# Optimization experiments

Measured on AMD Instinct MI355X. Metric: run time of the kernel, lower is better.

## Reference

```python
import jax, jax.numpy as jnp
import numpy as np

B, S, WIDTH, M = 2, 240, 128, 20
PAD = 16


def setup_inputs() -> dict:
    key = jax.random.key(0)
    ks = jax.random.split(key, 10)
    scale = 1.0 / (WIDTH * WIDTH)
    inp = {
        "x": jax.random.normal(ks[0], (B, S, S, 3), jnp.float32),
        "fc0_w": jax.random.normal(ks[1], (5, WIDTH), jnp.float32) * 0.1,
        "fc0_b": jnp.zeros((WIDTH,), jnp.float32),
        # 5 spectral layers, complex weights stored as [..., 2] = (real, imag)
        "spec_w1": jax.random.uniform(ks[2], (5, WIDTH, WIDTH, M, M, 2), jnp.float32) * scale,
        "spec_w2": jax.random.uniform(ks[3], (5, WIDTH, WIDTH, M, M, 2), jnp.float32) * scale,
        # 5 residual 1x1 convs
        "w_w": jax.random.normal(ks[4], (5, WIDTH, WIDTH), jnp.float32) / np.sqrt(WIDTH),
        "w_b": jnp.zeros((5, WIDTH), jnp.float32),
        "fc1_w": jax.random.normal(ks[5], (WIDTH, WIDTH), jnp.float32) / np.sqrt(WIDTH),
        "fc1_b": jnp.zeros((WIDTH,), jnp.float32),
        # 4 heads (u, v, p, T): width->64->1
        "head1_w": jax.random.normal(ks[6], (4, WIDTH, 64), jnp.float32) / np.sqrt(WIDTH),
        "head1_b": jnp.zeros((4, 64), jnp.float32),
        "head2_w": jax.random.normal(ks[7], (4, 64, 1), jnp.float32) / 8.0,
        "head2_b": jnp.zeros((4, 1), jnp.float32),
    }
    return inp


def _spectral_conv(h, w1, w2):
    # h: (B, C, H, W) real; w1, w2: (C_in, C_out, M, M) complex64
    Hh, Ww = h.shape[-2], h.shape[-1]
    ft = jnp.fft.rfft2(h)  # (B, C, H, W//2+1)
    o1 = jnp.einsum('bixy,ioxy->boxy', ft[:, :, :M, :M], w1)
    o2 = jnp.einsum('bixy,ioxy->boxy', ft[:, :, -M:, :M], w2)
    out_ft = jnp.zeros((h.shape[0], w1.shape[1], Hh, Ww // 2 + 1), jnp.complex64)
    out_ft = out_ft.at[:, :, :M, :M].set(o1).at[:, :, -M:, :M].set(o2)
    return jnp.fft.irfft2(out_ft, s=(Hh, Ww))


def reference(x, fc0_w, fc0_b, spec_w1, spec_w2, w_w, w_b, fc1_w, fc1_b,
              head1_w, head1_b, head2_w, head2_b):
    Bn, sx, sy = x.shape[0], x.shape[1], x.shape[2]
    gx = jnp.broadcast_to(jnp.linspace(0.0, 1.0, sx, dtype=x.dtype)[None, :, None, None], (Bn, sx, sy, 1))
    gy = jnp.broadcast_to(jnp.linspace(0.0, 1.0, sy, dtype=x.dtype)[None, None, :, None], (Bn, sx, sy, 1))
    x1 = jnp.concatenate([x, gx, gy], axis=-1)          # (B, S, S, 5)
    h = x1 @ fc0_w + fc0_b                              # lift -> (B, S, S, width)
    h = jnp.transpose(h, (0, 3, 1, 2))                  # (B, width, S, S)
    h = jnp.pad(h, ((0, 0), (0, 0), (0, PAD), (0, PAD)))
    c1 = spec_w1[..., 0] + 1j * spec_w1[..., 1]
    c2 = spec_w2[..., 0] + 1j * spec_w2[..., 1]
    for i in range(5):
        s = _spectral_conv(h, c1[i], c2[i])
        lin = jnp.einsum('bchw,oc->bohw', h, w_w[i]) + w_b[i][None, :, None, None]
        h = s + lin
        if i < 4:
            h = jax.nn.gelu(h, approximate=False)
    h = h[..., :-PAD, :-PAD]
    h = jnp.transpose(h, (0, 2, 3, 1))                  # (B, S, S, width)
    h = jax.nn.gelu(h @ fc1_w + fc1_b, approximate=False)
    h1 = jax.nn.gelu(jnp.einsum('bhwc,kcd->kbhwd', h, head1_w)
                     + head1_b[:, None, None, None, :], approximate=False)
    out = jnp.einsum('kbhwd,kdo->kbhwo', h1, head2_w) + head2_b[:, None, None, None, :]
    return (out[0], out[1], out[2], out[3])  # u, v, p, T each (B, S, S, 1)
```

## Files before the change

kernel.cpp:

```cpp
#include <hip/hip_runtime.h>
#include <math.h>


#define SZ_H   (2ull*256*256*128)
#define O_HA   0ull
#define O_HB   (O_HA + SZ_H)
#define O_G    (O_HB + SZ_H)
#define SZ_G   (2ull*256*20*128*2)
#define O_FTT  (O_G + SZ_G)
#define SZ_FT  (2ull*40*20*128*2)
#define O_OFT  (O_FTT + SZ_FT)
#define O_EY   (O_OFT + SZ_FT)
#define SZ_EY  (256ull*20*2)
#define O_EX   (O_EY + SZ_EY)
#define SZ_EX  (256ull*40*2)
#define O_EXI  (O_EX + SZ_EX)
#define O_WWT  (O_EXI + SZ_EX)
#define SZ_WWT 81920ull
#define O_PART (O_WWT + SZ_WWT)
#define SZ_PART (8ull*204800*2)

static __device__ __forceinline__ float gelu_f(float v) {
    return 0.5f * v * (1.0f + erff(v * 0.70710678118654752f));
}

__global__ void k_prep(const float* __restrict__ w_w, float* __restrict__ ws) {
    int i = blockIdx.x * 256 + threadIdx.x;
    const float STEP = 6.2831853071795864769f / 256.0f;
    if (i < 5120) {
        int ky = i % 20, y = i / 20;
        int t = (ky * y) & 255;
        float th = t * STEP;
        ws[O_EY + 2*(size_t)i]     = cosf(th);
        ws[O_EY + 2*(size_t)i + 1] = -sinf(th);
    } else if (i < 15360) {
        int m = i - 5120; int j = m % 40, x = m / 40;
        int kx = (j < 20) ? j : (216 + j);
        int t = (kx * x) & 255;
        float th = t * STEP;
        ws[O_EX + 2*(size_t)m]     = cosf(th);
        ws[O_EX + 2*(size_t)m + 1] = -sinf(th);
    } else if (i < 25600) {
        int m = i - 15360; int j = m % 40, x = m / 40;
        int kx = (j < 20) ? j : (216 + j);
        int t = (kx * x) & 255;
        float th = t * STEP;
        ws[O_EXI + 2*(size_t)m]     = cosf(th);
        ws[O_EXI + 2*(size_t)m + 1] = sinf(th);
    } else {
        int m = i - 25600;
        if (m < 81920) {
            int l = m >> 14, r = m & 16383;
            int ic = r >> 7, oc = r & 127;
            ws[O_WWT + m] = w_w[(size_t)l*16384 + oc*128 + ic];
        }
    }
}

__global__ __launch_bounds__(256) void k_fc0(const float* __restrict__ xin,
        const float* __restrict__ w, const float* __restrict__ bv,
        float4* __restrict__ H4) {
    size_t e = (size_t)blockIdx.x * 256 + threadIdx.x;
    int c4 = (int)(e & 31) * 4;
    int y = (int)((e >> 5) & 255);
    int x = (int)((e >> 13) & 255);
    int b = (int)(e >> 21);
    float4 h = make_float4(0.f, 0.f, 0.f, 0.f);
    if (x < 240 && y < 240) {
        const float* xp = xin + (((size_t)(b*240 + x))*240 + y)*3;
        float x0 = xp[0], x1 = xp[1], x2 = xp[2];
        float gx = x*(1.0f/239.0f), gy = y*(1.0f/239.0f);
        float4 w0 = *(const float4*)&w[c4];
        float4 w1 = *(const float4*)&w[128 + c4];
        float4 w2 = *(const float4*)&w[256 + c4];
        float4 w3 = *(const float4*)&w[384 + c4];
        float4 w4 = *(const float4*)&w[512 + c4];
        float4 bb = *(const float4*)&bv[c4];
        h.x = bb.x + x0*w0.x + x1*w1.x + x2*w2.x + gx*w3.x + gy*w4.x;
        h.y = bb.y + x0*w0.y + x1*w1.y + x2*w2.y + gx*w3.y + gy*w4.y;
        h.z = bb.z + x0*w0.z + x1*w1.z + x2*w2.z + gx*w3.z + gy*w4.z;
        h.w = bb.w + x0*w0.w + x1*w1.w + x2*w2.w + gx*w3.w + gy*w4.w;
    }
    H4[e] = h;
}

__global__ __launch_bounds__(256) void k_ydft(const float* __restrict__ H,
        const float* __restrict__ Ey, float2* __restrict__ G) {
    int kh = blockIdx.x & 1;
    int x  = (blockIdx.x >> 1) & 255;
    int b  = blockIdx.x >> 9;
    int c = threadIdx.x & 127;
    int yq = __builtin_amdgcn_readfirstlane((int)(threadIdx.x >> 7));
    int k0 = kh * 10;
    const float* Hrow = H + ((size_t)(b*256 + x)) * 256 * 128;
    float ar[10], ai[10];
    #pragma unroll
    for (int k = 0; k < 10; k++) { ar[k] = 0.f; ai[k] = 0.f; }
    #pragma unroll 2
    for (int i = 0; i < 128; i++) {
        int y = yq*128 + i;
        float v = Hrow[(size_t)y*128 + c];
        const float* e = Ey + (size_t)y*40 + k0*2;
        #pragma unroll
        for (int k = 0; k < 10; k++) {
            ar[k] = fmaf(v, e[2*k],   ar[k]);
            ai[k] = fmaf(v, e[2*k+1], ai[k]);
        }
    }
    __shared__ float red[10][128][2];
    if (yq == 1) {
        #pragma unroll
        for (int k = 0; k < 10; k++) { red[k][c][0] = ar[k]; red[k][c][1] = ai[k]; }
    }
    __syncthreads();
    if (yq == 0) {
        float2* Gp = G + ((size_t)(b*256 + x))*20*128;
        #pragma unroll
        for (int k = 0; k < 10; k++)
            Gp[(k0 + k)*128 + c] = make_float2(ar[k] + red[k][c][0], ai[k] + red[k][c][1]);
    }
}

__global__ __launch_bounds__(256) void k_xdft(const float2* __restrict__ G,
        const float* __restrict__ Ex, float2* __restrict__ ftT) {
    int t = blockIdx.x;
    int ch = t & 3, jq = (t >> 2) & 3, ky = (t >> 4) % 20, b = t / 320;
    int cl = threadIdx.x & 31;
    int xq = threadIdx.x >> 5;
    int c = ch*32 + cl;
    int j0 = jq*10;
    float ar[10], ai[10];
    #pragma unroll
    for (int k = 0; k < 10; k++) { ar[k] = 0.f; ai[k] = 0.f; }
    for (int i = 0; i < 32; i++) {
        int x = xq*32 + i;
        float2 g = G[(((size_t)(b*256 + x))*20 + ky)*128 + c];
        const float2* e2 = (const float2*)(Ex + (size_t)x*80) + j0;
        #pragma unroll
        for (int k = 0; k < 10; k++) {
            float2 e = e2[k];
            ar[k] = fmaf(g.x, e.x, fmaf(-g.y, e.y, ar[k]));
            ai[k] = fmaf(g.x, e.y, fmaf( g.y, e.x, ai[k]));
        }
    }
    #pragma unroll
    for (int k = 0; k < 10; k++) {
        ar[k] += __shfl_xor(ar[k], 32);
        ai[k] += __shfl_xor(ai[k], 32);
    }
    __shared__ float red[3][10][32][2];
    int wid = threadIdx.x >> 6;
    int sub = threadIdx.x & 63;
    if (wid > 0 && sub < 32) {
        #pragma unroll
        for (int k = 0; k < 10; k++) { red[wid-1][k][cl][0] = ar[k]; red[wid-1][k][cl][1] = ai[k]; }
    }
    __syncthreads();
    if (wid == 0 && sub < 32) {
        #pragma unroll
        for (int k = 0; k < 10; k++) {
            float rr = ar[k], ii = ai[k];
            #pragma unroll
            for (int q = 0; q < 3; q++) { rr += red[q][k][cl][0]; ii += red[q][k][cl][1]; }
            ftT[((size_t)c*2 + b)*800 + (size_t)(j0 + k)*20 + ky] = make_float2(rr, ii);
        }
    }
}

__global__ __launch_bounds__(448) void k_modemix(const float2* __restrict__ w1,
        const float2* __restrict__ w2, const float2* __restrict__ ftT,
        float2* __restrict__ outp, int ic_per) {
    int bid = blockIdx.x & 255;
    int icq = blockIdx.x >> 8;
    int oc = bid >> 1;
    int mh = bid & 1;
    int tid = threadIdx.x;
    if (tid >= 400) return;
    int wsel = tid / 200;
    int m = mh*200 + (tid % 200);
    int jk = wsel*400 + m;
    const float2* wb = wsel ? w2 : w1;
    int ic0 = icq * ic_per;
    float ar0=0.f, ai0=0.f, ar1=0.f, ai1=0.f;
    #pragma unroll 8
    for (int i = 0; i < ic_per; i++) {
        int ic = ic0 + i;
        float2 wv = wb[((size_t)(ic*128 + oc))*400 + m];
        float2 f0 = ftT[(size_t)ic*1600 + jk];
        float2 f1 = ftT[(size_t)ic*1600 + 800 + jk];
        ar0 = fmaf(f0.x, wv.x, fmaf(-f0.y, wv.y, ar0));
        ai0 = fmaf(f0.x, wv.y, fmaf( f0.y, wv.x, ai0));
        ar1 = fmaf(f1.x, wv.x, fmaf(-f1.y, wv.y, ar1));
        ai1 = fmaf(f1.x, wv.y, fmaf( f1.y, wv.x, ai1));
    }
    float2* o = outp + (size_t)icq * 204800;
    o[(size_t)jk*128 + oc]         = make_float2(ar0, ai0);
    o[(size_t)(800 + jk)*128 + oc] = make_float2(ar1, ai1);
}

__global__ __launch_bounds__(512) void k_modered(const float2* __restrict__ part,
        float2* __restrict__ oft) {
    int i = blockIdx.x * 512 + threadIdx.x;
    if (i >= 204800) return;
    float2 s = part[i];
    #pragma unroll
    for (int q = 1; q < 8; q++) {
        float2 p = part[(size_t)q*204800 + i];
        s.x += p.x; s.y += p.y;
    }
    oft[i] = s;
}

__global__ __launch_bounds__(256) void k_xidft(const float2* __restrict__ oft,
        const float* __restrict__ Exi, float2* __restrict__ T) {
    int kh = blockIdx.x & 1;
    int x  = (blockIdx.x >> 1) & 255;
    int b  = blockIdx.x >> 9;
    int oc = threadIdx.x & 127;
    int js = __builtin_amdgcn_readfirstlane((int)(threadIdx.x >> 7));
    int k0 = kh * 10;
    float ar[10], ai[10];
    #pragma unroll
    for (int k = 0; k < 10; k++) { ar[k] = 0.f; ai[k] = 0.f; }
    const float2* ob = oft + (size_t)b*800*128;
    for (int j = js*20; j < js*20 + 20; j++) {
        float er = Exi[(size_t)x*80 + 2*j], ei = Exi[(size_t)x*80 + 2*j + 1];
        #pragma unroll
        for (int k = 0; k < 10; k++) {
            float2 o = ob[(size_t)(j*20 + k0 + k)*128 + oc];
            ar[k] = fmaf(o.x, er, fmaf(-o.y, ei, ar[k]));
            ai[k] = fmaf(o.x, ei, fmaf( o.y, er, ai[k]));
        }
    }
    __shared__ float red[10][128][2];
    if (js == 1) {
        #pragma unroll
        for (int k = 0; k < 10; k++) { red[k][oc][0] = ar[k]; red[k][oc][1] = ai[k]; }
    }
    __syncthreads();
    if (js == 0) {
        float2* Tp = T + ((size_t)(b*256 + x))*20*128;
        #pragma unroll
        for (int k = 0; k < 10; k++)
            Tp[(k0 + k)*128 + oc] = make_float2(ar[k] + red[k][oc][0], ai[k] + red[k][oc][1]);
    }
}

__global__ __launch_bounds__(256) void k_spec_lin(const float* __restrict__ H,
        const float2* __restrict__ T, const float* __restrict__ wwT,
        const float* __restrict__ wb, float* __restrict__ Hout, int do_gelu) {
    int yg = blockIdx.x & 3;
    int x  = (blockIdx.x >> 2) & 255;
    int b  = blockIdx.x >> 10;
    int tid = threadIdx.x;
    int lane = tid & 63;
    int wv = __builtin_amdgcn_readfirstlane(tid >> 6);
    int oc0 = wv * 32;
    int y0 = yg * 64;
    __shared__ float hl[64][132];
    const float* Hbase = H + (((size_t)(b*256 + x))*256 + y0)*128;
    #pragma unroll
    for (int it = 0; it < 8; it++) {
        int i = tid + it*256;
        int pi = i >> 5, c4 = (i & 31)*4;
        float4 v = *(const float4*)&Hbase[(size_t)pi*128 + c4];
        *(float4*)&hl[pi][c4] = v;
    }
    __syncthreads();
    float acc[32];
    #pragma unroll
    for (int o = 0; o < 32; o++) acc[o] = 0.f;
    for (int icb = 0; icb < 128; icb += 16) {
        float tvals[16];
        #pragma unroll
        for (int q = 0; q < 4; q++)
            *(float4*)&tvals[q*4] = *(const float4*)&hl[lane][icb + q*4];
        #pragma unroll
        for (int ii = 0; ii < 16; ii++) {
            float t = tvals[ii];
            const float* wr = &wwT[(size_t)(icb + ii)*128 + oc0];
            #pragma unroll
            for (int o4 = 0; o4 < 8; o4++) {
                float4 w = *(const float4*)&wr[o4*4];
                acc[o4*4]   = fmaf(t, w.x, acc[o4*4]);
                acc[o4*4+1] = fmaf(t, w.y, acc[o4*4+1]);
                acc[o4*4+2] = fmaf(t, w.z, acc[o4*4+2]);
                acc[o4*4+3] = fmaf(t, w.w, acc[o4*4+3]);
            }
        }
    }
    float csr[20], csi[20];
    {
        int y = y0 + lane;
        #pragma unroll
        for (int k = 0; k < 20; k++) {
            int t = (k * y) & 255;
            float th = t * (6.2831853071795864769f/256.0f);
            float f = (k == 0 ? 1.0f : 2.0f) * (1.0f/65536.0f);
            csr[k] = f * __cosf(th);
            csi[k] = f * __sinf(th);
        }
    }
    const float2* Tp = T + ((size_t)(b*256 + x))*20*128 + oc0;
    for (int k = 0; k < 20; k++) {
        const float2* tr = Tp + (size_t)k*128;
        float cr = csr[k], ci = csi[k];
        #pragma unroll
        for (int o = 0; o < 32; o++) {
            float2 tv = tr[o];
            acc[o] = fmaf(tv.x, cr, fmaf(-tv.y, ci, acc[o]));
        }
    }
    __syncthreads();
    const float* bp = &wb[oc0];
    #pragma unroll
    for (int o4 = 0; o4 < 8; o4++) {
        float4 r;
        r.x = acc[o4*4]   + bp[o4*4];
        r.y = acc[o4*4+1] + bp[o4*4+1];
        r.z = acc[o4*4+2] + bp[o4*4+2];
        r.w = acc[o4*4+3] + bp[o4*4+3];
        if (do_gelu) { r.x = gelu_f(r.x); r.y = gelu_f(r.y); r.z = gelu_f(r.z); r.w = gelu_f(r.w); }
        *(float4*)&hl[lane][oc0 + o4*4] = r;
    }
    __syncthreads();
    float* Obase = Hout + (((size_t)(b*256 + x))*256 + y0)*128;
    #pragma unroll
    for (int it = 0; it < 32; it++) {
        int i = tid + it*256;
        int pi = i >> 7, c = i & 127;
        Obase[(size_t)pi*128 + c] = hl[pi][c];
    }
}

__global__ __launch_bounds__(512) void k_tail(const float* __restrict__ H,
        const float* __restrict__ fc1_w, const float* __restrict__ fc1_b,
        const float* __restrict__ h1w, const float* __restrict__ h1b,
        const float* __restrict__ h2w, const float* __restrict__ h2b,
        float* __restrict__ out) {
    int tid = threadIdx.x;
    int lane = tid & 63;
    int wv = __builtin_amdgcn_readfirstlane(tid >> 6);
    int p0 = blockIdx.x * 64;
    __shared__ float smem[64*132];
    __shared__ float red[4][64];
    float (*hl)[132] = (float (*)[132])smem;
    #pragma unroll
    for (int it = 0; it < 4; it++) {
        int i = tid + it*512;
        int pi = i >> 5, c4 = (i & 31)*4;
        int p = p0 + pi;
        int bb = p / 57600, r = p % 57600;
        int xx = r / 240, yy = r % 240;
        float4 v = *(const float4*)&H[(((size_t)(bb*256 + xx))*256 + yy)*128 + c4];
        *(float4*)&hl[pi][c4] = v;
    }
    __syncthreads();
    int oc0 = wv * 16;
    float acc[16];
    #pragma unroll
    for (int o = 0; o < 16; o++) acc[o] = 0.f;
    for (int icb = 0; icb < 128; icb += 16) {
        float tvals[16];
        #pragma unroll
        for (int q = 0; q < 4; q++)
            *(float4*)&tvals[q*4] = *(const float4*)&hl[lane][icb + q*4];
        #pragma unroll
        for (int ii = 0; ii < 16; ii++) {
            float t = tvals[ii];
            const float* wr = &fc1_w[(size_t)(icb + ii)*128 + oc0];
            #pragma unroll
            for (int o4 = 0; o4 < 4; o4++) {
                float4 w = *(const float4*)&wr[o4*4];
                acc[o4*4]   = fmaf(t, w.x, acc[o4*4]);
                acc[o4*4+1] = fmaf(t, w.y, acc[o4*4+1]);
                acc[o4*4+2] = fmaf(t, w.z, acc[o4*4+2]);
                acc[o4*4+3] = fmaf(t, w.w, acc[o4*4+3]);
            }
        }
    }
    __syncthreads();
    #pragma unroll
    for (int o4 = 0; o4 < 4; o4++) {
        float4 bb = *(const float4*)&fc1_b[oc0 + o4*4];
        float4 r;
        r.x = gelu_f(acc[o4*4]   + bb.x);
        r.y = gelu_f(acc[o4*4+1] + bb.y);
        r.z = gelu_f(acc[o4*4+2] + bb.z);
        r.w = gelu_f(acc[o4*4+3] + bb.w);
        *(float4*)&hl[lane][oc0 + o4*4] = r;
    }
    __syncthreads();
    int k    = wv >> 1;
    int half = wv & 1;
    int d0 = half * 32;
    float a2[32];
    #pragma unroll
    for (int d = 0; d < 32; d++) a2[d] = 0.f;
    const float* wk = h1w + (size_t)k*8192 + d0;
    for (int cb = 0; cb < 128; cb += 8) {
        float tvals[8];
        *(float4*)&tvals[0] = *(const float4*)&hl[lane][cb];
        *(float4*)&tvals[4] = *(const float4*)&hl[lane][cb + 4];
        #pragma unroll
        for (int cc = 0; cc < 8; cc++) {
            float t = tvals[cc];
            const float* wr = &wk[(cb + cc)*64];
            #pragma unroll
            for (int d4 = 0; d4 < 8; d4++) {
                float4 w = *(const float4*)&wr[d4*4];
                a2[d4*4]   = fmaf(t, w.x, a2[d4*4]);
                a2[d4*4+1] = fmaf(t, w.y, a2[d4*4+1]);
                a2[d4*4+2] = fmaf(t, w.z, a2[d4*4+2]);
                a2[d4*4+3] = fmaf(t, w.w, a2[d4*4+3]);
            }
        }
    }
    const float* b1 = &h1b[k*64 + d0];
    const float* w2 = &h2w[k*64 + d0];
    float ph = 0.f;
    #pragma unroll
    for (int d = 0; d < 32; d++)
        ph += gelu_f(a2[d] + b1[d]) * w2[d];
    if (half == 1) red[k][lane] = ph;
    __syncthreads();
    if (half == 0)
        out[(size_t)k*115200 + p0 + lane] = ph + red[k][lane] + h2b[k];
}

extern "C" void kernel_launch(void* const* d_in, const int* in_sizes, int n_in,
                              void* d_out, int out_size, void* d_ws, size_t ws_size,
                              hipStream_t stream) {
    const float* x       = (const float*)d_in[0];
    const float* fc0_w   = (const float*)d_in[1];
    const float* fc0_b   = (const float*)d_in[2];
    const float* spec_w1 = (const float*)d_in[3];
    const float* spec_w2 = (const float*)d_in[4];
    const float* w_w     = (const float*)d_in[5];
    const float* w_b     = (const float*)d_in[6];
    const float* fc1_w   = (const float*)d_in[7];
    const float* fc1_b   = (const float*)d_in[8];
    const float* head1_w = (const float*)d_in[9];
    const float* head1_b = (const float*)d_in[10];
    const float* head2_w = (const float*)d_in[11];
    const float* head2_b = (const float*)d_in[12];
    float* ws = (float*)d_ws;
    float* out = (float*)d_out;

    int split = ws_size >= (size_t)(O_PART + SZ_PART) * 4 ? 1 : 0;

    k_prep<<<420, 256, 0, stream>>>(w_w, ws);
    k_fc0<<<16384, 256, 0, stream>>>(x, fc0_w, fc0_b, (float4*)(ws + O_HA));

    float* cur = ws + O_HA;
    float* nxt = ws + O_HB;
    float2* G    = (float2*)(ws + O_G);
    float2* ftT  = (float2*)(ws + O_FTT);
    float2* oft  = (float2*)(ws + O_OFT);
    float2* part = (float2*)(ws + O_PART);

    for (int l = 0; l < 5; l++) {
        k_ydft<<<1024, 256, 0, stream>>>(cur, ws + O_EY, G);
        k_xdft<<<640, 256, 0, stream>>>(G, ws + O_EX, ftT);
        const float2* w1l = (const float2*)(spec_w1 + (size_t)l*13107200);
        const float2* w2l = (const float2*)(spec_w2 + (size_t)l*13107200);
        if (split) {
            k_modemix<<<2048, 448, 0, stream>>>(w1l, w2l, ftT, part, 16);
            k_modered<<<400, 512, 0, stream>>>(part, oft);
        } else {
            k_modemix<<<256, 448, 0, stream>>>(w1l, w2l, ftT, oft, 128);
        }
        k_xidft<<<1024, 256, 0, stream>>>(oft, ws + O_EXI, G);
        k_spec_lin<<<2048, 256, 0, stream>>>(cur, G, ws + O_WWT + (size_t)l*16384,
                                             w_b + l*128, nxt, (l < 4) ? 1 : 0);
        float* t = cur; cur = nxt; nxt = t;
    }
    k_tail<<<1800, 512, 0, stream>>>(cur, fc1_w, fc1_b, head1_w, head1_b,
                                     head2_w, head2_b, out);
}
```

Measured before the change: 1.726 ms.

## Restructure ydft, spec_lin and tail kernels with LDS-staged twiddles and swizzled transposes

The y-DFT kernel now stages its twiddle table in shared memory and has each thread handle two channels over four y-quarters, adding a two-step shared-memory reduction and writing float4 results. The spectral+linear kernel moves to 512 threads. It stores the input tile transposed in shared memory with an XOR swizzle, so each thread owns one output channel across 16 positions and reads one weight per input channel instead of float4 weight vectors. It also reuses the precomputed Ey table for inverse-y twiddles instead of computing sin/cos, and writes results directly from registers. The tail kernel gets the same swizzled transpose plus a shuffle-based head reduction, trading more shared-memory traffic and extra barriers for fewer global weight loads and better coalescing.

```diff
diff --git a/kernel.cpp b/kernel.cpp
--- a/kernel.cpp
+++ b/kernel.cpp
@@ -22,6 +22,10 @@
 
 static __device__ __forceinline__ float gelu_f(float v) {
     return 0.5f * v * (1.0f + erff(v * 0.70710678118654752f));
+}
+
+static __device__ __forceinline__ int SWZ(int row, int col) {
+    return (row << 6) | ((((col >> 2) ^ ((row >> 2) & 15)) << 2) | (col & 3));
 }
 
 __global__ void k_prep(const float* __restrict__ w_w, float* __restrict__ ws) {
@@ -89,35 +93,66 @@
     int kh = blockIdx.x & 1;
     int x  = (blockIdx.x >> 1) & 255;
     int b  = blockIdx.x >> 9;
-    int c = threadIdx.x & 127;
-    int yq = __builtin_amdgcn_readfirstlane((int)(threadIdx.x >> 7));
+    int lane = threadIdx.x & 63;
+    int yq = __builtin_amdgcn_readfirstlane((int)(threadIdx.x >> 6));
     int k0 = kh * 10;
-    const float* Hrow = H + ((size_t)(b*256 + x)) * 256 * 128;
-    float ar[10], ai[10];
-    #pragma unroll
-    for (int k = 0; k < 10; k++) { ar[k] = 0.f; ai[k] = 0.f; }
+    __shared__ float2 eyl[256][10];
+    __shared__ float4 red[2][10][64];
+    for (int i = threadIdx.x; i < 2560; i += 256) {
+        int y = i / 10, kk = i - y*10;
+        eyl[y][kk] = *(const float2*)&Ey[(size_t)y*40 + (size_t)(k0 + kk)*2];
+    }
+    __syncthreads();
+    const float* Hrow = H + ((size_t)(b*256 + x))*256*128 + 2*lane;
+    float ar0[10], ai0[10], ar1[10], ai1[10];
+    #pragma unroll
+    for (int k = 0; k < 10; k++) { ar0[k]=0.f; ai0[k]=0.f; ar1[k]=0.f; ai1[k]=0.f; }
     #pragma unroll 2
-    for (int i = 0; i < 128; i++) {
-        int y = yq*128 + i;
-        float v = Hrow[(size_t)y*128 + c];
-        const float* e = Ey + (size_t)y*40 + k0*2;
+    for (int yi = 0; yi < 64; yi++) {
+        int y = yq*64 + yi;
+        float2 h = *(const float2*)&Hrow[(size_t)y*128];
+        float4 ev[5];
+        const float4* ep = (const float4*)&eyl[y][0];
+        #pragma unroll
+        for (int q = 0; q < 5; q++) ev[q] = ep[q];
+        const float2* e2p = (const float2*)&ev[0];
         #pragma unroll
         for (int k = 0; k < 10; k++) {
-            ar[k] = fmaf(v, e[2*k],   ar[k]);
-            ai[k] = fmaf(v, e[2*k+1], ai[k]);
-        }
-    }
-    __shared__ float red[10][128][2];
+            float2 e = e2p[k];
+            ar0[k] = fmaf(h.x, e.x, ar0[k]);
+            ai0[k] = fmaf(h.x, e.y, ai0[k]);
+            ar1[k] = fmaf(h.y, e.x, ar1[k]);
+            ai1[k] = fmaf(h.y, e.y, ai1[k]);
+        }
+    }
+    if (yq >= 2) {
+        #pragma unroll
+        for (int k = 0; k < 10; k++)
+            red[yq-2][k][lane] = make_float4(ar0[k], ai0[k], ar1[k], ai1[k]);
+    }
+    __syncthreads();
+    if (yq < 2) {
+        #pragma unroll
+        for (int k = 0; k < 10; k++) {
+            float4 r = red[yq][k][lane];
+            ar0[k]+=r.x; ai0[k]+=r.y; ar1[k]+=r.z; ai1[k]+=r.w;
+        }
+    }
+    __syncthreads();
     if (yq == 1) {
         #pragma unroll
-        for (int k = 0; k < 10; k++) { red[k][c][0] = ar[k]; red[k][c][1] = ai[k]; }
+        for (int k = 0; k < 10; k++)
+            red[0][k][lane] = make_float4(ar0[k], ai0[k], ar1[k], ai1[k]);
     }
     __syncthreads();
     if (yq == 0) {
-        float2* Gp = G + ((size_t)(b*256 + x))*20*128;
-        #pragma unroll
-        for (int k = 0; k < 10; k++)
-            Gp[(k0 + k)*128 + c] = make_float2(ar[k] + red[k][c][0], ai[k] + red[k][c][1]);
+        float2* Gp = G + ((size_t)(b*256 + x))*20*128 + 2*lane;
+        #pragma unroll
+        for (int k = 0; k < 10; k++) {
+            float4 r = red[0][k][lane];
+            float4 o = make_float4(ar0[k]+r.x, ai0[k]+r.y, ar1[k]+r.z, ai1[k]+r.w);
+            *(float4*)&Gp[(size_t)(k0 + k)*128] = o;
+        }
     }
 }
 
@@ -246,90 +281,88 @@
     }
 }
 
-__global__ __launch_bounds__(256) void k_spec_lin(const float* __restrict__ H,
+__global__ __launch_bounds__(512) void k_spec_lin(const float* __restrict__ H,
         const float2* __restrict__ T, const float* __restrict__ wwT,
-        const float* __restrict__ wb, float* __restrict__ Hout, int do_gelu) {
+        const float* __restrict__ wb, const float* __restrict__ Ey,
+        float* __restrict__ Hout, int do_gelu) {
     int yg = blockIdx.x & 3;
     int x  = (blockIdx.x >> 2) & 255;
     int b  = blockIdx.x >> 10;
     int tid = threadIdx.x;
     int lane = tid & 63;
     int wv = __builtin_amdgcn_readfirstlane(tid >> 6);
-    int oc0 = wv * 32;
     int y0 = yg * 64;
-    __shared__ float hl[64][132];
+    __shared__ __align__(16) float smem[128*64];
+    __shared__ float2 csl[20][64];
     const float* Hbase = H + (((size_t)(b*256 + x))*256 + y0)*128;
     #pragma unroll
-    for (int it = 0; it < 8; it++) {
-        int i = tid + it*256;
+    for (int it = 0; it < 4; it++) {
+        int i = tid + it*512;
         int pi = i >> 5, c4 = (i & 31)*4;
         float4 v = *(const float4*)&Hbase[(size_t)pi*128 + c4];
-        *(float4*)&hl[pi][c4] = v;
-    }
-    __syncthreads();
-    float acc[32];
-    #pragma unroll
-    for (int o = 0; o < 32; o++) acc[o] = 0.f;
-    for (int icb = 0; icb < 128; icb += 16) {
-        float tvals[16];
-        #pragma unroll
-        for (int q = 0; q < 4; q++)
-            *(float4*)&tvals[q*4] = *(const float4*)&hl[lane][icb + q*4];
-        #pragma unroll
-        for (int ii = 0; ii < 16; ii++) {
-            float t = tvals[ii];
-            const float* wr = &wwT[(size_t)(icb + ii)*128 + oc0];
-            #pragma unroll
-            for (int o4 = 0; o4 < 8; o4++) {
-                float4 w = *(const float4*)&wr[o4*4];
-                acc[o4*4]   = fmaf(t, w.x, acc[o4*4]);
-                acc[o4*4+1] = fmaf(t, w.y, acc[o4*4+1]);
-                acc[o4*4+2] = fmaf(t, w.z, acc[o4*4+2]);
-                acc[o4*4+3] = fmaf(t, w.w, acc[o4*4+3]);
-            }
-        }
-    }
-    float csr[20], csi[20];
-    {
-        int y = y0 + lane;
-        #pragma unroll
-        for (int k = 0; k < 20; k++) {
-            int t = (k * y) & 255;
-            float th = t * (6.2831853071795864769f/256.0f);
-            float f = (k == 0 ? 1.0f : 2.0f) * (1.0f/65536.0f);
-            csr[k] = f * __cosf(th);
-            csi[k] = f * __sinf(th);
-        }
-    }
-    const float2* Tp = T + ((size_t)(b*256 + x))*20*128 + oc0;
+        smem[SWZ(c4+0, pi)] = v.x;
+        smem[SWZ(c4+1, pi)] = v.y;
+        smem[SWZ(c4+2, pi)] = v.z;
+        smem[SWZ(c4+3, pi)] = v.w;
+    }
+    for (int i = tid; i < 1280; i += 512) {
+        int k = i >> 6, yl = i & 63;
+        float2 e = *(const float2*)&Ey[(size_t)(y0 + yl)*40 + (size_t)k*2];
+        float f = (k == 0 ? 1.0f : 2.0f) * (1.0f/65536.0f);
+        csl[k][yl] = make_float2(f*e.x, -f*e.y);
+    }
+    __syncthreads();
+    int yq = wv >> 1, oh = wv & 1;
+    int oc = oh*64 + lane;
+    int yb = yq * 16;
+    int cb0 = yb >> 2;
+    float acc[16];
+    #pragma unroll
+    for (int o = 0; o < 16; o++) acc[o] = 0.f;
+    #pragma unroll 4
+    for (int ic = 0; ic < 128; ic++) {
+        float w = wwT[(size_t)ic*128 + oc];
+        const float* row = &smem[ic << 6];
+        int g = (ic >> 2) & 15;
+        float4 a0 = *(const float4*)&row[((cb0+0) ^ g) << 2];
+        float4 a1 = *(const float4*)&row[((cb0+1) ^ g) << 2];
+        float4 a2v = *(const float4*)&row[((cb0+2) ^ g) << 2];
+        float4 a3 = *(const float4*)&row[((cb0+3) ^ g) << 2];
+        acc[0]  = fmaf(a0.x,  w, acc[0]);
+        acc[1]  = fmaf(a0.y,  w, acc[1]);
+        acc[2]  = fmaf(a0.z,  w, acc[2]);
+        acc[3]  = fmaf(a0.w,  w, acc[3]);
+        acc[4]  = fmaf(a1.x,  w, acc[4]);
+        acc[5]  = fmaf(a1.y,  w, acc[5]);
+        acc[6]  = fmaf(a1.z,  w, acc[6]);
+        acc[7]  = fmaf(a1.w,  w, acc[7]);
+        acc[8]  = fmaf(a2v.x, w, acc[8]);
+        acc[9]  = fmaf(a2v.y, w, acc[9]);
+        acc[10] = fmaf(a2v.z, w, acc[10]);
+        acc[11] = fmaf(a2v.w, w, acc[11]);
+        acc[12] = fmaf(a3.x,  w, acc[12]);
+        acc[13] = fmaf(a3.y,  w, acc[13]);
+        acc[14] = fmaf(a3.z,  w, acc[14]);
+        acc[15] = fmaf(a3.w,  w, acc[15]);
+    }
+    const float2* Tp = T + ((size_t)(b*256 + x))*20*128;
     for (int k = 0; k < 20; k++) {
-        const float2* tr = Tp + (size_t)k*128;
-        float cr = csr[k], ci = csi[k];
-        #pragma unroll
-        for (int o = 0; o < 32; o++) {
-            float2 tv = tr[o];
-            acc[o] = fmaf(tv.x, cr, fmaf(-tv.y, ci, acc[o]));
-        }
-    }
-    __syncthreads();
-    const float* bp = &wb[oc0];
-    #pragma unroll
-    for (int o4 = 0; o4 < 8; o4++) {
-        float4 r;
-        r.x = acc[o4*4]   + bp[o4*4];
-        r.y = acc[o4*4+1] + bp[o4*4+1];
-        r.z = acc[o4*4+2] + bp[o4*4+2];
-        r.w = acc[o4*4+3] + bp[o4*4+3];
-        if (do_gelu) { r.x = gelu_f(r.x); r.y = gelu_f(r.y); r.z = gelu_f(r.z); r.w = gelu_f(r.w); }
-        *(float4*)&hl[lane][oc0 + o4*4] = r;
-    }
-    __syncthreads();
+        float2 tv = Tp[(size_t)k*128 + oc];
+        const float4* cp = (const float4*)&csl[k][yb];
+        #pragma unroll
+        for (int j = 0; j < 8; j++) {
+            float4 cs2 = cp[j];
+            acc[2*j]   = fmaf(tv.x, cs2.x, fmaf(-tv.y, cs2.y, acc[2*j]));
+            acc[2*j+1] = fmaf(tv.x, cs2.z, fmaf(-tv.y, cs2.w, acc[2*j+1]));
+        }
+    }
+    float bv = wb[oc];
     float* Obase = Hout + (((size_t)(b*256 + x))*256 + y0)*128;
     #pragma unroll
-    for (int it = 0; it < 32; it++) {
-        int i = tid + it*256;
-        int pi = i >> 7, c = i & 127;
-        Obase[(size_t)pi*128 + c] = hl[pi][c];
+    for (int p = 0; p < 16; p++) {
+        float v = acc[p] + bv;
+        if (do_gelu) v = gelu_f(v);
+        Obase[(size_t)(yb + p)*128 + oc] = v;
     }
 }
 
@@ -342,9 +375,7 @@
     int lane = tid & 63;
     int wv = __builtin_amdgcn_readfirstlane(tid >> 6);
     int p0 = blockIdx.x * 64;
-    __shared__ float smem[64*132];
-    __shared__ float red[4][64];
-    float (*hl)[132] = (float (*)[132])smem;
+    __shared__ __align__(16) float smem[128*64];
     #pragma unroll
     for (int it = 0; it < 4; it++) {
         int i = tid + it*512;
@@ -353,79 +384,82 @@
         int bb = p / 57600, r = p % 57600;
         int xx = r / 240, yy = r % 240;
         float4 v = *(const float4*)&H[(((size_t)(bb*256 + xx))*256 + yy)*128 + c4];
-        *(float4*)&hl[pi][c4] = v;
-    }
-    __syncthreads();
-    int oc0 = wv * 16;
+        smem[SWZ(c4+0, pi)] = v.x;
+        smem[SWZ(c4+1, pi)] = v.y;
+        smem[SWZ(c4+2, pi)] = v.z;
+        smem[SWZ(c4+3, pi)] = v.w;
+    }
+    __syncthreads();
+    int pg = wv >> 1, half = wv & 1;
+    int oc = half*64 + lane;
+    int yb = pg * 16;
+    int cb0 = yb >> 2;
     float acc[16];
     #pragma unroll
     for (int o = 0; o < 16; o++) acc[o] = 0.f;
-    for (int icb = 0; icb < 128; icb += 16) {
-        float tvals[16];
-        #pragma unroll
-        for (int q = 0; q < 4; q++)
-            *(float4*)&tvals[q*4] = *(const float4*)&hl[lane][icb + q*4];
-        #pragma unroll
-        for (int ii = 0; ii < 16; ii++) {
-            float t = tvals[ii];
-            const float* wr = &fc1_w[(size_t)(icb + ii)*128 + oc0];
-            #pragma unroll
-            for (int o4 = 0; o4 < 4; o4++) {
-                float4 w = *(const float4*)&wr[o4*4];
-                acc[o4*4]   = fmaf(t, w.x, acc[o4*4]);
-                acc[o4*4+1] = fmaf(t, w.y, acc[o4*4+1]);
-                acc[o4*4+2] = fmaf(t, w.z, acc[o4*4+2]);
-                acc[o4*4+3] = fmaf(t, w.w, acc[o4*4+3]);
-            }
-        }
-    }
-    __syncthreads();
-    #pragma unroll
-    for (int o4 = 0; o4 < 4; o4++) {
-        float4 bb = *(const float4*)&fc1_b[oc0 + o4*4];
-        float4 r;
-        r.x = gelu_f(acc[o4*4]   + bb.x);
-        r.y = gelu_f(acc[o4*4+1] + bb.y);
-        r.z = gelu_f(acc[o4*4+2] + bb.z);
-        r.w = gelu_f(acc[o4*4+3] + bb.w);
-        *(float4*)&hl[lane][oc0 + o4*4] = r;
-    }
-    __syncthreads();
-    int k    = wv >> 1;
-    int half = wv & 1;
-    int d0 = half * 32;
+    #pragma unroll 4
+    for (int ic = 0; ic < 128; ic++) {
+        float w = fc1_w[(size_t)ic*128 + oc];
+        const float* row = &smem[ic << 6];
+        int g = (ic >> 2) & 15;
+        float4 a0 = *(const float4*)&row[((cb0+0) ^ g) << 2];
+        float4 a1 = *(const float4*)&row[((cb0+1) ^ g) << 2];
+        float4 a2v = *(const float4*)&row[((cb0+2) ^ g) << 2];
+        float4 a3 = *(const float4*)&row[((cb0+3) ^ g) << 2];
+        acc[0]  = fmaf(a0.x,  w, acc[0]);
+        acc[1]  = fmaf(a0.y,  w, acc[1]);
+        acc[2]  = fmaf(a0.z,  w, acc[2]);
+        acc[3]  = fmaf(a0.w,  w, acc[3]);
+        acc[4]  = fmaf(a1.x,  w, acc[4]);
+        acc[5]  = fmaf(a1.y,  w, acc[5]);
+        acc[6]  = fmaf(a1.z,  w, acc[6]);
+        acc[7]  = fmaf(a1.w,  w, acc[7]);
+        acc[8]  = fmaf(a2v.x, w, acc[8]);
+        acc[9]  = fmaf(a2v.y, w, acc[9]);
+        acc[10] = fmaf(a2v.z, w, acc[10]);
+        acc[11] = fmaf(a2v.w, w, acc[11]);
+        acc[12] = fmaf(a3.x,  w, acc[12]);
+        acc[13] = fmaf(a3.y,  w, acc[13]);
+        acc[14] = fmaf(a3.z,  w, acc[14]);
+        acc[15] = fmaf(a3.w,  w, acc[15]);
+    }
+    __syncthreads();
+    {
+        float bb = fc1_b[oc];
+        #pragma unroll
+        for (int p = 0; p < 16; p++)
+            smem[SWZ(oc, yb + p)] = gelu_f(acc[p] + bb);
+    }
+    __syncthreads();
+    int hk = wv & 3, ph = wv >> 2;
+    int px = ph*32 + (lane >> 1);
+    int d0 = (lane & 1) * 32;
     float a2[32];
     #pragma unroll
     for (int d = 0; d < 32; d++) a2[d] = 0.f;
-    const float* wk = h1w + (size_t)k*8192 + d0;
-    for (int cb = 0; cb < 128; cb += 8) {
-        float tvals[8];
-        *(float4*)&tvals[0] = *(const float4*)&hl[lane][cb];
-        *(float4*)&tvals[4] = *(const float4*)&hl[lane][cb + 4];
-        #pragma unroll
-        for (int cc = 0; cc < 8; cc++) {
-            float t = tvals[cc];
-            const float* wr = &wk[(cb + cc)*64];
-            #pragma unroll
-            for (int d4 = 0; d4 < 8; d4++) {
-                float4 w = *(const float4*)&wr[d4*4];
-                a2[d4*4]   = fmaf(t, w.x, a2[d4*4]);
-                a2[d4*4+1] = fmaf(t, w.y, a2[d4*4+1]);
-                a2[d4*4+2] = fmaf(t, w.z, a2[d4*4+2]);
-                a2[d4*4+3] = fmaf(t, w.w, a2[d4*4+3]);
-            }
-        }
-    }
-    const float* b1 = &h1b[k*64 + d0];
-    const float* w2 = &h2w[k*64 + d0];
-    float ph = 0.f;
+    const float* wk = h1w + (size_t)hk*8192 + d0;
+    #pragma unroll 2
+    for (int c = 0; c < 128; c++) {
+        float t = smem[SWZ(c, px)];
+        const float4* wp = (const float4*)&wk[(size_t)c*64];
+        #pragma unroll
+        for (int j = 0; j < 8; j++) {
+            float4 w = wp[j];
+            a2[j*4+0] = fmaf(t, w.x, a2[j*4+0]);
+            a2[j*4+1] = fmaf(t, w.y, a2[j*4+1]);
+            a2[j*4+2] = fmaf(t, w.z, a2[j*4+2]);
+            a2[j*4+3] = fmaf(t, w.w, a2[j*4+3]);
+        }
+    }
+    float s = 0.f;
+    const float* b1 = &h1b[hk*64 + d0];
+    const float* w2 = &h2w[hk*64 + d0];
     #pragma unroll
     for (int d = 0; d < 32; d++)
-        ph += gelu_f(a2[d] + b1[d]) * w2[d];
-    if (half == 1) red[k][lane] = ph;
-    __syncthreads();
-    if (half == 0)
-        out[(size_t)k*115200 + p0 + lane] = ph + red[k][lane] + h2b[k];
+        s += gelu_f(a2[d] + b1[d]) * w2[d];
+    s += __shfl_xor(s, 1);
+    if ((lane & 1) == 0)
+        out[(size_t)hk*115200 + p0 + px] = s + h2b[hk];
 }
 
 extern "C" void kernel_launch(void* const* d_in, const int* in_sizes, int n_in,
@@ -471,8 +505,9 @@
             k_modemix<<<256, 448, 0, stream>>>(w1l, w2l, ftT, oft, 128);
         }
         k_xidft<<<1024, 256, 0, stream>>>(oft, ws + O_EXI, G);
-        k_spec_lin<<<2048, 256, 0, stream>>>(cur, G, ws + O_WWT + (size_t)l*16384,
-                                             w_b + l*128, nxt, (l < 4) ? 1 : 0);
+        k_spec_lin<<<2048, 512, 0, stream>>>(cur, G, ws + O_WWT + (size_t)l*16384,
+                                             w_b + l*128, ws + O_EY, nxt,
+                                             (l < 4) ? 1 : 0);
         float* t = cur; cur = nxt; nxt = t;
     }
     k_tail<<<1800, 512, 0, stream>>>(cur, fc1_w, fc1_b, head1_w, head1_b,
```

Measured after the change: 6.832 ms. 3.96x slower.
